# Kernel tuning notes

Measured on AMD Instinct MI355X. Metric: run time of the kernel, lower is better.

## Reference

```python
import jax, jax.numpy as jnp
import numpy as np

B, T, H, NH, DH, R = 2, 2048, 1024, 16, 64, 256
ALPHA = 0.6


def setup_inputs() -> dict:
    key = jax.random.key(0)
    ks = jax.random.split(key, 28)
    f32 = jnp.float32

    def nrm(k, shape, s=0.02):
        return jax.random.normal(k, shape, dtype=f32) * s

    inp = {}
    inp['x'] = jax.random.normal(ks[0], (B, T, H), dtype=f32)
    # additive causal mask [1,1,T,T]: 0 on/below diagonal, -1e9 above
    causal = jnp.tril(jnp.ones((T, T), dtype=bool))
    inp['attention_mask'] = jnp.where(causal, 0.0, -1e9).astype(f32)[None, None]
    # low-rank SVD factors for q,k,v,o: Vh [H,R], S [R] (positive), U [H,R], b [H]
    i = 1
    for name in ('q', 'k', 'v', 'o'):
        inp['Vh_' + name] = nrm(ks[i], (H, R)); i += 1
        inp['S_' + name] = jax.random.uniform(ks[i], (R,), dtype=f32, minval=0.5, maxval=1.5); i += 1
        inp['U_' + name] = nrm(ks[i], (H, R)); i += 1
        inp['b_' + name] = jnp.zeros((H,), dtype=f32); i += 1
    # full-rank weights of the original (fallback) attention: y = x @ W + b (Conv1D style)
    for name in ('q', 'k', 'v', 'o'):
        inp['W_' + name] = nrm(ks[i], (H, H)); i += 1
        inp['bf_' + name] = jnp.zeros((H,), dtype=f32); i += 1
    return inp


def _split_heads(t):
    # [B,T,H] -> [B,nH,T,dH]
    Bs, Ts, _ = t.shape
    return t.reshape(Bs, Ts, NH, DH).transpose(0, 2, 1, 3)


def _attention(Q, K, V, mask):
    q, k, v = _split_heads(Q), _split_heads(K), _split_heads(V)
    scores = jnp.einsum('bhtd,bhsd->bhts', q, k) / (DH ** 0.5)
    scores = scores + mask
    w = jax.nn.softmax(scores, axis=-1)
    ctx = jnp.einsum('bhts,bhsd->bhtd', w, v)
    Bs = ctx.shape[0]
    return ctx.transpose(0, 2, 1, 3).reshape(Bs, -1, NH * DH)


def _lowrank(x, Vh, S, U, b):
    # ((x @ Vh) * S) @ U.T + b
    return ((x @ Vh) * S) @ U.T + b


def reference(x, attention_mask,
              Vh_q, S_q, U_q, b_q, Vh_k, S_k, U_k, b_k,
              Vh_v, S_v, U_v, b_v, Vh_o, S_o, U_o, b_o,
              W_q, bf_q, W_k, bf_k, W_v, bf_v, W_o, bf_o):
    # --- low-rank SVD path ---
    Q = _lowrank(x, Vh_q, S_q, U_q, b_q)
    K = _lowrank(x, Vh_k, S_k, U_k, b_k)
    V = _lowrank(x, Vh_v, S_v, U_v, b_v)
    ctx = _attention(Q, K, V, attention_mask)
    out = _lowrank(ctx, Vh_o, S_o, U_o, b_o)
    # --- fallback: original full-rank attention ---
    Qf = x @ W_q + bf_q
    Kf = x @ W_k + bf_k
    Vf = x @ W_v + bf_v
    ctxf = _attention(Qf, Kf, Vf, attention_mask)
    fallback_out = ctxf @ W_o + bf_o
    return ALPHA * out + (1.0 - ALPHA) * fallback_out
```

## Files before the change

### kernel.cpp

```cpp
#include <hip/hip_runtime.h>
#include <hip/hip_bf16.h>

typedef __bf16 bf16_t;
typedef __bf16 bf16x8 __attribute__((ext_vector_type(8)));
typedef float f32x4 __attribute__((ext_vector_type(4)));
typedef _Float16 f16_t;
typedef _Float16 f16x4 __attribute__((ext_vector_type(4)));

extern "C" __device__ float __ocml_native_exp2_f32(float);

#define DEVI static __device__ __forceinline__

static constexpr int TN   = 2048;
static constexpr int Hn   = 1024;
static constexpr int Rn   = 256;
static constexpr int MTOK = 4096;
static constexpr int NCAT = 6144;

static constexpr float QSCALE = 0.125f;
static constexpr float LOG2E  = 1.44269504088896340736f;
static constexpr float SOFT_OFF2 = 0.426950408889634f;

template <typename T>
DEVI void gload16(const T* g, T* l) {
    __builtin_amdgcn_global_load_lds(
        (const __attribute__((address_space(1))) void*)g,
        (__attribute__((address_space(3))) void*)l, 16, 0, 0);
}

DEVI float loadf(const void* base, int idx, bool bfm) {
    if (bfm) {
        unsigned int u = ((const unsigned short*)base)[idx];
        u <<= 16;
        return __builtin_bit_cast(float, u);
    }
    return ((const float*)base)[idx];
}
DEVI bool detect_bf16(const void* mask) {
    return fabsf(((const float*)mask)[0]) > 1.0f;
}

struct PrepArgs {
    const void *x, *mask;
    const void *Vh[4], *S[4], *U[4];
    const void *bb[4], *bfb[4];
    bf16_t *Xb, *Abuf, *Bbuf;
    float *biascat, *biaso;
};

__global__ void k_prep(PrepArgs a) {
    const bool bfm = detect_bf16(a.mask);
    const int bid = blockIdx.x;
    if (bid < 4096) {
        int i = (bid * 256 + threadIdx.x) * 4;
#pragma unroll
        for (int j = 0; j < 4; ++j) a.Xb[i + j] = (bf16_t)loadf(a.x, i + j, bfm);
    } else if (bid < 8192) {
        int idx = (bid - 4096) * 256 + threadIdx.x;
        int proj = idx >> 18;
        int e = idx & 262143;
        int r = e & 255;
        float s = loadf(a.S[proj], r, bfm);
        if (proj == 0) s *= QSCALE * LOG2E;
        if (proj == 3) s *= 0.6f;
        a.Abuf[idx] = (bf16_t)(loadf(a.U[proj], e, bfm) * s);
        a.Bbuf[idx] = (bf16_t)loadf(a.Vh[proj], e, bfm);
    } else {
        int i = (bid - 8192) * 256 + threadIdx.x;
        if (i < 1024)      a.biascat[i] = QSCALE * LOG2E * loadf(a.bb[0], i, bfm);
        else if (i < 2048) a.biascat[i] = loadf(a.bb[1], i - 1024, bfm);
        else if (i < 3072) a.biascat[i] = loadf(a.bb[2], i - 2048, bfm);
        else if (i < 4096) a.biascat[i] = QSCALE * LOG2E * loadf(a.bfb[0], i - 3072, bfm);
        else if (i < 5120) a.biascat[i] = loadf(a.bfb[1], i - 4096, bfm);
        else if (i < 6144) a.biascat[i] = loadf(a.bfb[2], i - 5120, bfm);
        else {
            int j = i - 6144;
            a.biaso[j] = 0.6f * loadf(a.bb[3], j, bfm) + 0.4f * loadf(a.bfb[3], j, bfm);
        }
    }
}

struct TransP { const void* W[4]; bf16_t* dst[4]; int ldd[4]; float scale[4]; const void* mask; };

__global__ void k_transpose4(TransP tp) {
    const bool bfm = detect_bf16(tp.mask);
    const int z = blockIdx.z;
    const void* W = tp.W[z];
    bf16_t* dst = tp.dst[z];
    const int ldd = tp.ldd[z];
    const float scale = tp.scale[z];
    __shared__ float t[32][33];
    int bx = blockIdx.x * 32, by = blockIdx.y * 32;
    int tx = threadIdx.x, ty = threadIdx.y;
#pragma unroll
    for (int k = 0; k < 32; k += 8)
        t[ty + k][tx] = loadf(W, (by + ty + k) * Hn + bx + tx, bfm);
    __syncthreads();
#pragma unroll
    for (int k = 0; k < 32; k += 8)
        dst[(size_t)(bx + ty + k) * ldd + by + tx] = (bf16_t)(scale * t[tx][ty + k]);
}

template <int MI>
DEVI void gemm_core64(const bf16_t* __restrict__ A, int lda,
                      const bf16_t* __restrict__ B, int ldb, int K,
                      bf16_t* A0, bf16_t* A1, bf16_t* B0, bf16_t* B1,
                      int bm, int bn, f32x4 (&acc)[MI][4]) {
    constexpr int MT = MI * 32;
    const int tid  = threadIdx.x;
    const int lane = tid & 63;
    const int w    = tid >> 6;
    const int wr   = (w >> 1) * (MI * 16);
    const int wc   = (w & 1) * 64;
    const int fr   = lane & 15;
    const int quad = lane >> 4;

#pragma unroll
    for (int i = 0; i < MI; ++i)
#pragma unroll
        for (int j = 0; j < 4; ++j) acc[i][j] = {0.f, 0.f, 0.f, 0.f};

    for (int kb = 0; kb < K; kb += 64) {
        __syncthreads();
        for (int u = tid; u < MT * 4; u += 256) {
            const bf16_t* as = &A[(size_t)(bm + (u >> 2)) * lda + kb + (u & 3) * 8];
            gload16(as,      &A0[u * 8]);
            gload16(as + 32, &A1[u * 8]);
        }
#pragma unroll
        for (int t = 0; t < 2; ++t) {
            int u = t * 256 + tid;
            const bf16_t* bs = &B[(size_t)(bn + (u >> 2)) * ldb + kb + (u & 3) * 8];
            gload16(bs,      &B0[u * 8]);
            gload16(bs + 32, &B1[u * 8]);
        }
        __syncthreads();

#pragma unroll
        for (int kk = 0; kk < 2; ++kk) {
            const bf16_t* Ap = kk ? A1 : A0;
            const bf16_t* Bp = kk ? B1 : B0;
            bf16x8 af[MI], bfv[4];
#pragma unroll
            for (int i = 0; i < MI; ++i)
                af[i] = *(const bf16x8*)&Ap[(wr + i * 16 + fr) * 32 + quad * 8];
#pragma unroll
            for (int j = 0; j < 4; ++j)
                bfv[j] = *(const bf16x8*)&Bp[(wc + j * 16 + fr) * 32 + quad * 8];
#pragma unroll
            for (int i = 0; i < MI; ++i)
#pragma unroll
                for (int j = 0; j < 4; ++j)
                    acc[i][j] = __builtin_amdgcn_mfma_f32_16x16x32_bf16(af[i], bfv[j], acc[i][j], 0, 0, 0);
        }
    }
}

template <int MI, bool OUT_DUAL, bool WRITE_VT>
__global__ __launch_bounds__(256)
void k_gemm(const bf16_t* __restrict__ A, int lda,
            const bf16_t* __restrict__ B, int ldb,
            void* __restrict__ C, int ldc, int K,
            const float* __restrict__ bias, const void* __restrict__ mask,
            f16_t* __restrict__ Vt_g) {
    constexpr int MT = MI * 32;
    struct GB { bf16_t A0[MT * 32]; bf16_t A1[MT * 32]; bf16_t B0[4096]; bf16_t B1[4096]; };
    union SM { GB g; f16_t Ls[WRITE_VT ? 128 * 136 : 8]; };
    __shared__ __align__(16) SM sm;

    const int tid  = threadIdx.x;
    const int lane = tid & 63;
    const int w    = tid >> 6;
    const int wr   = (w >> 1) * (MI * 16);
    const int wc   = (w & 1) * 64;
    const int bm   = blockIdx.x * MT;
    const int bn   = blockIdx.y * 128;
    const int fr   = lane & 15;
    const int quad = lane >> 4;

    f32x4 acc[MI][4];
    gemm_core64<MI>(A, lda, B, ldb, K, sm.g.A0, sm.g.A1, sm.g.B0, sm.g.B1, bm, bn, acc);

    if constexpr (WRITE_VT) {
        const bool isV = (bn >= 2048 && bn < 3072) || (bn >= 5120);
        if (isV) {
            const int pth = (bn >= 5120) ? 1 : 0;
            const int colrel = bn - (pth ? 5120 : 2048);
            const int bb = bm >> 11;
            const int R0 = (pth * 32 + bb * 16 + (colrel >> 6)) * 64;
            const int tloc = bm & 2047;
            __syncthreads();
#pragma unroll
            for (int i = 0; i < MI; ++i) {
                const int t0 = wr + i * 16 + quad * 4;
#pragma unroll
                for (int j = 0; j < 4; ++j) {
                    const int c = wc + j * 16 + fr;
                    const float bv = bias[bn + c];
#pragma unroll
                    for (int r = 0; r < 4; ++r)
                        sm.Ls[c * 136 + t0 + r] = (f16_t)(acc[i][j][r] + bv);
                }
            }
            __syncthreads();
            const int c = tid >> 1, seg = tid & 1;
            f16_t* dst = &Vt_g[(size_t)(R0 + c) * TN + tloc + seg * 64];
            const f16_t* src = &sm.Ls[c * 136 + seg * 64];
#pragma unroll
            for (int e = 0; e < 8; ++e)
                *(uint4*)&dst[e * 8] = *(const uint4*)&src[e * 8];
            return;
        }
    }

    bool bfm = false;
    if constexpr (OUT_DUAL) bfm = detect_bf16(mask);
#pragma unroll
    for (int i = 0; i < MI; ++i) {
        const int row0 = bm + wr + i * 16 + quad * 4;
#pragma unroll
        for (int j = 0; j < 4; ++j) {
            const int col = bn + wc + j * 16 + fr;
            const float bv = bias ? bias[col] : 0.f;
#pragma unroll
            for (int r = 0; r < 4; ++r) {
                float v = acc[i][j][r] + bv;
                size_t ci = (size_t)(row0 + r) * ldc + col;
                if constexpr (OUT_DUAL) {
                    if (bfm) ((unsigned short*)C)[ci] = __builtin_bit_cast(unsigned short, (bf16_t)v);
                    else     ((float*)C)[ci] = v;
                } else {
                    ((bf16_t*)C)[ci] = (bf16_t)v;
                }
            }
        }
    }
}

__global__ __launch_bounds__(256)
void k_gemm_small4(const bf16_t* __restrict__ Abuf, const bf16_t* __restrict__ Bbuf,
                   bf16_t* __restrict__ Wcat, bf16_t* __restrict__ WoT) {
    __shared__ __align__(16) bf16_t A0[64 * 32], A1[64 * 32], B0[4096], B1[4096];
    const int z = blockIdx.z;
    const bf16_t* A = Abuf + (size_t)z * Hn * Rn;
    const bf16_t* B = Bbuf + (size_t)z * Hn * Rn;
    bf16_t* C = (z < 3) ? (Wcat + (size_t)z * Hn * Hn) : WoT;
    const int ldc = (z < 3) ? Hn : 2048;

    const int bm = blockIdx.x * 64, bn = blockIdx.y * 128;
    f32x4 acc[2][4];
    gemm_core64<2>(A, Rn, B, Rn, Rn, A0, A1, B0, B1, bm, bn, acc);

    const int lane = threadIdx.x & 63;
    const int w    = threadIdx.x >> 6;
    const int wr   = (w >> 1) * 32;
    const int wc   = (w & 1) * 64;
    const int fr   = lane & 15;
    const int quad = lane >> 4;
#pragma unroll
    for (int i = 0; i < 2; ++i)
#pragma unroll
        for (int j = 0; j < 4; ++j)
#pragma unroll
            for (int r = 0; r < 4; ++r)
                C[(size_t)(bm + wr + i * 16 + quad * 4 + r) * ldc + bn + wc + j * 16 + fr]
                    = (bf16_t)acc[i][j][r];
}

__global__ __launch_bounds__(256, 4)
void k_flash6(const bf16_t* __restrict__ Y, const f16_t* __restrict__ Vt_g,
              bf16_t* __restrict__ Ctx) {
    const int id   = blockIdx.x;
    const int inst = id & 63;
    const int slot = (id >> 6) & 3;
    const int rnd  = id >> 8;
    const int qt2  = (rnd == 0) ? 15 - slot
                   : (rnd == 1) ? 11 - slot
                   : (rnd == 2) ? 4 + slot
                                : slot;
    const int p = inst >> 5, b = (inst >> 4) & 1, h = inst & 15;

    const int tid  = threadIdx.x;
    const int lane = tid & 63;
    const int w    = tid >> 6;
    const int fr   = lane & 15;
    const int quad = lane >> 4;

    const int rowbase = b * TN;
    const int qbase   = qt2 * 128;
    const int qcol = p * 3072 + h * 64;
    const int kcol = qcol + 1024;
    const int ccol = p * 1024 + h * 64;

    __shared__ __align__(16) bf16_t Kb[2][2][64 * 32];
    __shared__ __align__(16) f16_t  Vb[2][64 * 64];

    const int r64 = tid >> 2;
    const int c8s = (((tid & 3) ^ ((tid >> 4) & 3)) * 8);
    const int ksw = (quad ^ ((fr >> 2) & 3)) * 8;

    size_t vsrc[2];
#pragma unroll
    for (int t = 0; t < 2; ++t) {
        int pp = w * 128 + t * 64 + lane;
        int d  = pp >> 3;
        vsrc[t] = (size_t)(inst * 64 + d) * TN + ((((pp & 7) - d) & 7) * 8);
    }

    f16x4 ones;
#pragma unroll
    for (int j = 0; j < 4; ++j) ones[j] = (f16_t)1.0f;

    const f32x4 off4 = {-SOFT_OFF2, -SOFT_OFF2, -SOFT_OFF2, -SOFT_OFF2};

    bf16x8 qf[2][2];
#pragma unroll
    for (int s = 0; s < 2; ++s) {
        const size_t qrow = (size_t)(rowbase + qbase + s * 64 + w * 16 + fr) * NCAT + qcol;
        qf[s][0] = *(const bf16x8*)&Y[qrow + quad * 8];
        qf[s][1] = *(const bf16x8*)&Y[qrow + 32 + quad * 8];
    }

    f32x4 o[2][4], lacc[2];
#pragma unroll
    for (int s = 0; s < 2; ++s) {
        lacc[s] = {0.f, 0.f, 0.f, 0.f};
#pragma unroll
        for (int db = 0; db < 4; ++db) o[s][db] = {0.f, 0.f, 0.f, 0.f};
    }

    const int t0 = (quad >> 1) + (fr & 7);
    const int h4 = (quad & 1) * 4;
    int voff[4];
#pragma unroll
    for (int nb = 0; nb < 4; ++nb) voff[nb] = ((nb * 2 + t0) & 7) * 8;

    const int kl = quad * 4;
    const int ql = w * 16 + fr;

    const int kmax = 2 * qt2 + 1;

    auto stage = [&](int kt, int bsel) {
        const bf16_t* ksrc = &Y[(size_t)(rowbase + kt * 64 + r64) * NCAT + kcol + c8s];
        gload16(ksrc,      &Kb[bsel][0][tid * 8]);
        gload16(ksrc + 32, &Kb[bsel][1][tid * 8]);
#pragma unroll
        for (int t = 0; t < 2; ++t)
            gload16(&Vt_g[vsrc[t] + kt * 64], &Vb[bsel][(w * 128 + t * 64 + lane) * 8]);
    };

    stage(0, 0);

    for (int kt = 0; kt <= kmax; ++kt) {
        const int cur = kt & 1;
        __syncthreads();
        if (kt < kmax) stage(kt + 1, cur ^ 1);

        const bool a0 = (kt < kmax);

        f16x4 pf[2][4];
#pragma unroll
        for (int nb = 0; nb < 4; ++nb) {
            const int ka = (nb * 16 + fr) * 32 + ksw;
            bf16x8 kf0 = *(const bf16x8*)&Kb[cur][0][ka];
            bf16x8 kf1 = *(const bf16x8*)&Kb[cur][1][ka];
#pragma unroll
            for (int s = 0; s < 2; ++s) {
                if (s == 0 && !a0) continue;
                f32x4 t4 = __builtin_amdgcn_mfma_f32_16x16x32_bf16(kf0, qf[s][0], off4, 0, 0, 0);
                t4 = __builtin_amdgcn_mfma_f32_16x16x32_bf16(kf1, qf[s][1], t4, 0, 0, 0);
                if (kt == 2 * qt2 + s) {
#pragma unroll
                    for (int r = 0; r < 4; ++r)
                        if (nb * 16 + kl + r > ql) t4[r] = -1e30f;
                }
                auto lo = __builtin_amdgcn_cvt_pkrtz(__ocml_native_exp2_f32(t4[0]),
                                                     __ocml_native_exp2_f32(t4[1]));
                auto hi = __builtin_amdgcn_cvt_pkrtz(__ocml_native_exp2_f32(t4[2]),
                                                     __ocml_native_exp2_f32(t4[3]));
                pf[s][nb] = __builtin_bit_cast(f16x4, __builtin_shufflevector(lo, hi, 0, 1, 2, 3));
            }
        }

#pragma unroll
        for (int s = 0; s < 2; ++s) {
            if (s == 0 && !a0) continue;
#pragma unroll
            for (int nb = 0; nb < 4; ++nb)
                lacc[s] = __builtin_amdgcn_mfma_f32_16x16x16f16(pf[s][nb], ones, lacc[s], 0, 0, 0);
        }

#pragma unroll
        for (int db = 0; db < 4; ++db) {
            const int vbase = (db * 16 + fr) * 64 + h4;
            f16x4 vf[4];
#pragma unroll
            for (int nb = 0; nb < 4; ++nb)
                vf[nb] = *(const f16x4*)&Vb[cur][vbase + voff[nb]];
#pragma unroll
            for (int nb = 0; nb < 4; ++nb) {
                o[1][db] = __builtin_amdgcn_mfma_f32_16x16x16f16(pf[1][nb], vf[nb], o[1][db], 0, 0, 0);
                if (a0)
                    o[0][db] = __builtin_amdgcn_mfma_f32_16x16x16f16(pf[0][nb], vf[nb], o[0][db], 0, 0, 0);
            }
        }
    }

#pragma unroll
    for (int s = 0; s < 2; ++s)
#pragma unroll
        for (int r = 0; r < 4; ++r) {
            const float inv = 1.0f / lacc[s][r];
            const size_t trow = (size_t)(rowbase + qbase + s * 64 + w * 16 + quad * 4 + r);
#pragma unroll
            for (int db = 0; db < 4; ++db)
                Ctx[trow * 2048 + ccol + db * 16 + fr] = (bf16_t)(o[s][db][r] * inv);
        }
}

extern "C" void kernel_launch(void* const* d_in, const int* in_sizes, int n_in,
                              void* d_out, int out_size, void* d_ws, size_t ws_size,
                              hipStream_t stream) {
    const void* x    = d_in[0];
    const void* mask = d_in[1];
    const void* Vh[4] = { d_in[2],  d_in[6],  d_in[10], d_in[14] };
    const void* Sp[4] = { d_in[3],  d_in[7],  d_in[11], d_in[15] };
    const void* Up[4] = { d_in[4],  d_in[8],  d_in[12], d_in[16] };
    const void* bb[4] = { d_in[5],  d_in[9],  d_in[13], d_in[17] };
    const void* Wp[4] = { d_in[18], d_in[20], d_in[22], d_in[24] };
    const void* bf[4] = { d_in[19], d_in[21], d_in[23], d_in[25] };

    char* ws = (char*)d_ws;
    size_t off = 0;
    auto alloc = [&](size_t bytes) -> void* {
        void* p = ws + off;
        off = (off + bytes + 255) & ~(size_t)255;
        return p;
    };
    bf16_t* Xb      = (bf16_t*)alloc((size_t)MTOK * Hn * 2);
    bf16_t* Wcat    = (bf16_t*)alloc((size_t)NCAT * Hn * 2);
    bf16_t* Yb      = (bf16_t*)alloc((size_t)MTOK * NCAT * 2);
    bf16_t* Ctx     = (bf16_t*)alloc((size_t)MTOK * 2048 * 2);
    bf16_t* WoT     = (bf16_t*)alloc((size_t)Hn * 2048 * 2);
    f16_t*  Vt_g    = (f16_t*)alloc((size_t)64 * 64 * TN * 2);
    bf16_t* Abuf    = (bf16_t*)alloc((size_t)4 * Hn * Rn * 2);
    bf16_t* Bbuf    = (bf16_t*)alloc((size_t)4 * Hn * Rn * 2);
    float*  biascat = (float*)alloc(NCAT * 4);
    float*  biaso   = (float*)alloc(Hn * 4);

    PrepArgs pa;
    pa.x = x; pa.mask = mask;
    for (int i = 0; i < 4; ++i) {
        pa.Vh[i] = Vh[i]; pa.S[i] = Sp[i]; pa.U[i] = Up[i];
        pa.bb[i] = bb[i]; pa.bfb[i] = bf[i];
    }
    pa.Xb = Xb; pa.Abuf = Abuf; pa.Bbuf = Bbuf; pa.biascat = biascat; pa.biaso = biaso;
    k_prep<<<8220, 256, 0, stream>>>(pa);

    TransP tp;
    for (int i = 0; i < 3; ++i) {
        tp.W[i] = Wp[i]; tp.dst[i] = Wcat + (size_t)(3 * Hn + i * Hn) * Hn;
        tp.ldd[i] = Hn; tp.scale[i] = (i == 0) ? QSCALE * LOG2E : 1.0f;
    }
    tp.W[3] = Wp[3]; tp.dst[3] = WoT + 1024; tp.ldd[3] = 2048; tp.scale[3] = 0.4f;
    tp.mask = mask;
    k_transpose4<<<dim3(32, 32, 4), dim3(32, 8), 0, stream>>>(tp);

    k_gemm_small4<<<dim3(16, 8, 4), 256, 0, stream>>>(Abuf, Bbuf, Wcat, WoT);

    k_gemm<4, false, true><<<dim3(32, 48), 256, 0, stream>>>(
        Xb, Hn, Wcat, Hn, Yb, NCAT, Hn, biascat, nullptr, Vt_g);

    k_flash6<<<1024, 256, 0, stream>>>(Yb, Vt_g, Ctx);

    k_gemm<2, true, false><<<dim3(64, 8), 256, 0, stream>>>(
        Ctx, 2048, WoT, 2048, d_out, Hn, 2048, biaso, mask, nullptr);
}
```

Baseline: 290.1 us.

## Replace QKV projection GEMM with 256x128-tile 8-wave pipelined kernel

Adds a new GEMM kernel for the fused QKV projection (4096x6144x1024). It uses 512 threads, 256x128 output tiles and a double-buffered K=64 pipeline with swizzled LDS and explicit vmcnt waits. It also uses an XCD-aware block remap, s_setprio around the MFMA bursts, and an LDS-transposed fp16 store for the V columns. The aim is more operand reuse per tile and better overlap of global loads with MFMAs, at the cost of higher register and LDS pressure and hand-tuned wait counts that must stay correct.

```diff
diff --git a/kernel.cpp b/kernel.cpp
--- a/kernel.cpp
+++ b/kernel.cpp
@@ -237,6 +237,130 @@
     }
 }
 
+__global__ __launch_bounds__(512, 2)
+void k_gemm8(const bf16_t* __restrict__ A, int lda,
+             const bf16_t* __restrict__ B, int ldb,
+             bf16_t* __restrict__ C, int ldc, int K,
+             const float* __restrict__ bias, f16_t* __restrict__ Vt_g) {
+    struct Pipe { bf16_t At[2][2][256 * 32]; bf16_t Bt[2][2][128 * 32]; };
+    union SM8 { Pipe p; f16_t Ls[128 * 264]; };
+    __shared__ __align__(16) SM8 sm;
+
+    const int tid  = threadIdx.x;
+    const int lane = tid & 63;
+    const int wid  = tid >> 6;
+    const int wr   = (wid >> 1) * 64;
+    const int wc   = (wid & 1) * 64;
+    const int fr   = lane & 15;
+    const int quad = lane >> 4;
+
+    const int bid = blockIdx.x;
+    const int sz  = (bid & 7) * 96 + (bid >> 3);
+    const int bm  = (sz & 15) * 256;
+    const int bn  = (sz >> 4) * 128;
+
+    const int csrc = ((tid & 3) ^ ((tid >> 3) & 3)) * 8;
+    const int ksw  = (quad ^ ((fr >> 1) & 3)) * 8;
+    const int raB  = (wr + fr) * 32 + ksw;
+    const int rbB  = (wc + fr) * 32 + ksw;
+    const int r0   = tid >> 2;
+
+    auto stage = [&](int t, int kk) {
+        const int bufi = t & 1;
+        const int kb = t * 64 + kk * 32;
+        gload16(&A[(size_t)(bm + r0) * lda + kb + csrc],       &sm.p.At[bufi][kk][tid * 8]);
+        gload16(&A[(size_t)(bm + 128 + r0) * lda + kb + csrc], &sm.p.At[bufi][kk][(512 + tid) * 8]);
+        gload16(&B[(size_t)(bn + r0) * ldb + kb + csrc],       &sm.p.Bt[bufi][kk][tid * 8]);
+    };
+
+    f32x4 acc[4][4];
+#pragma unroll
+    for (int i = 0; i < 4; ++i)
+#pragma unroll
+        for (int j = 0; j < 4; ++j) acc[i][j] = {0.f, 0.f, 0.f, 0.f};
+
+    const int NT = K >> 6;
+    stage(0, 0);
+    stage(0, 1);
+
+    for (int t = 0; t < NT; ++t) {
+        const int cur = t & 1;
+#pragma unroll
+        for (int kk = 0; kk < 2; ++kk) {
+            if (t + 1 < NT) {
+                stage(t + 1, kk);
+                asm volatile("s_waitcnt vmcnt(6)" ::: "memory");
+            } else if (kk == 0) {
+                asm volatile("s_waitcnt vmcnt(3)" ::: "memory");
+            } else {
+                asm volatile("s_waitcnt vmcnt(0)" ::: "memory");
+            }
+            __builtin_amdgcn_s_barrier();
+            __builtin_amdgcn_sched_barrier(0);
+
+            bf16x8 af[4], bv[4];
+#pragma unroll
+            for (int i = 0; i < 4; ++i)
+                af[i] = *(const bf16x8*)&sm.p.At[cur][kk][raB + i * 512];
+#pragma unroll
+            for (int j = 0; j < 4; ++j)
+                bv[j] = *(const bf16x8*)&sm.p.Bt[cur][kk][rbB + j * 512];
+
+            __builtin_amdgcn_s_setprio(1);
+#pragma unroll
+            for (int i = 0; i < 4; ++i)
+#pragma unroll
+                for (int j = 0; j < 4; ++j)
+                    acc[i][j] = __builtin_amdgcn_mfma_f32_16x16x32_bf16(af[i], bv[j], acc[i][j], 0, 0, 0);
+            __builtin_amdgcn_s_setprio(0);
+        }
+    }
+
+    const bool isV = (bn >= 2048 && bn < 3072) || (bn >= 5120);
+    if (isV) {
+        const int pth = (bn >= 5120) ? 1 : 0;
+        const int pbase = pth ? 5120 : 2048;
+        const int bb = bm >> 11;
+        const int vrow0 = (pth * 32 + bb * 16) * 64 + (bn - pbase);
+        const int tloc = bm & 2047;
+        __syncthreads();
+#pragma unroll
+        for (int j = 0; j < 4; ++j) {
+            const int c = wc + j * 16 + fr;
+            const float bv = bias[bn + c];
+#pragma unroll
+            for (int i = 0; i < 4; ++i) {
+                const int t0 = wr + i * 16 + quad * 4;
+                f16x4 pk;
+#pragma unroll
+                for (int r = 0; r < 4; ++r) pk[r] = (f16_t)(acc[i][j][r] + bv);
+                *(f16x4*)&sm.Ls[c * 264 + t0] = pk;
+            }
+        }
+        __syncthreads();
+        const int c = tid >> 2, seg = tid & 3;
+        f16_t* dst = &Vt_g[(size_t)(vrow0 + c) * TN + tloc + seg * 64];
+        const f16_t* src = &sm.Ls[c * 264 + seg * 64];
+#pragma unroll
+        for (int e = 0; e < 8; ++e)
+            *(uint4*)&dst[e * 8] = *(const uint4*)&src[e * 8];
+        return;
+    }
+
+#pragma unroll
+    for (int i = 0; i < 4; ++i) {
+        const int row0 = bm + wr + i * 16 + quad * 4;
+#pragma unroll
+        for (int j = 0; j < 4; ++j) {
+            const int col = bn + wc + j * 16 + fr;
+            const float bv = bias[col];
+#pragma unroll
+            for (int r = 0; r < 4; ++r)
+                C[(size_t)(row0 + r) * ldc + col] = (bf16_t)(acc[i][j][r] + bv);
+        }
+    }
+}
+
 __global__ __launch_bounds__(256)
 void k_gemm_small4(const bf16_t* __restrict__ Abuf, const bf16_t* __restrict__ Bbuf,
                    bf16_t* __restrict__ Wcat, bf16_t* __restrict__ WoT) {
@@ -468,8 +592,8 @@
 
     k_gemm_small4<<<dim3(16, 8, 4), 256, 0, stream>>>(Abuf, Bbuf, Wcat, WoT);
 
-    k_gemm<4, false, true><<<dim3(32, 48), 256, 0, stream>>>(
-        Xb, Hn, Wcat, Hn, Yb, NCAT, Hn, biascat, nullptr, Vt_g);
+    k_gemm8<<<768, 512, 0, stream>>>(
+        Xb, Hn, Wcat, Hn, Yb, NCAT, Hn, biascat, Vt_g);
 
     k_flash6<<<1024, 256, 0, stream>>>(Yb, Vt_g, Ctx);
 
```

Result: slower. 308.6 us (+6.4%).
